# Optimization experiments

Measured on AMD Instinct MI355X. Metric: run time of the kernel, lower is better.

The kernel has to match this reference:

```python
import jax, jax.numpy as jnp
import numpy as np
from jax import lax

G, N, S, K, R = 8, 4096, 2048, 64, 0.4   # graphs, nodes/graph, fps samples (ratio=0.5), max neighbors, radius
EPER = 65536                              # edges per graph (avg degree 16)
C = 13                                    # num_classes


def setup_inputs():
    key = jax.random.key(0)
    ks = jax.random.split(key, 8)
    norm = jax.random.normal(ks[0], (G * N, 3), jnp.float32)
    pos = jax.random.uniform(ks[1], (G * N, 3), jnp.float32)
    x = jax.random.normal(ks[2], (G * N, 2), jnp.float32)
    e = jax.random.randint(ks[3], (2, G, EPER), 0, N)
    off = (jnp.arange(G) * N)[None, :, None]
    edge_index = (e + off).reshape(2, G * EPER).astype(jnp.int64)
    batch = jnp.repeat(jnp.arange(G), N).astype(jnp.int64)
    def lin(k, i, o):
        return jax.random.normal(k, (i, o), jnp.float32) / np.float32(np.sqrt(i))
    W1 = lin(ks[4], 8, 64);    b1 = jnp.zeros((64,), jnp.float32)
    W2 = lin(ks[5], 72, 128);  b2 = jnp.zeros((128,), jnp.float32)
    W3 = lin(ks[6], 139, 256); b3 = jnp.zeros((256,), jnp.float32)
    lin_w = lin(ks[7], 256, C); lin_b = jnp.zeros((C,), jnp.float32)
    return dict(norm=norm, pos=pos, x=x, edge_index=edge_index, batch=batch,
                W1=W1, b1=b1, W2=W2, b2=b2, W3=W3, b3=b3, lin_w=lin_w, lin_b=lin_b)


def _gcn(h, src, dst, ew, W, b, n):
    # GCNConv(normalize=False): out[dst] += ew * (h @ W)[src]; + bias
    m = (h @ W)[src] * ew[:, None]
    return jax.ops.segment_sum(m, dst, num_segments=n) + b


def _fps(p):  # farthest point sampling on one graph, p: [N,3] -> [S] local indices (start at node 0)
    def step(carry, _):
        mind, cur = carry
        d = jnp.sum((p - p[cur]) ** 2, axis=1)
        mind = jnp.minimum(mind, d)
        return (mind, jnp.argmax(mind).astype(jnp.int32)), cur
    _, idx = lax.scan(step, (jnp.full((N,), jnp.inf, p.dtype), jnp.int32(0)), None, length=S)
    return idx


def _radius(p, q):  # p [N,3], q [S,3] -> neighbor cols [S,K] (lowest-index-first within radius), valid mask
    d2 = jnp.sum((q[:, None, :] - p[None, :, :]) ** 2, axis=-1)  # [S,N]
    mask = d2 < R * R
    score = jnp.where(mask, N - jnp.arange(N, dtype=jnp.int32)[None, :], 0)
    vals, cols = lax.top_k(score, K)
    valid = vals > 0
    return jnp.where(valid, cols, 0), valid


def reference(norm, pos, x, edge_index, batch, W1, b1, W2, b2, W3, b3, lin_w, lin_b):
    NT = G * N
    inp = jnp.concatenate([norm, pos, x], axis=1)          # [NT, 8]
    src, dst = edge_index[0], edge_index[1]
    ew = jnp.ones((src.shape[0],), inp.dtype)
    # dropout is inactive at inference (training=False)
    h1 = jax.nn.relu(_gcn(inp, src, dst, ew, W1, b1, NT))  # [NT, 64]
    h1 = jnp.concatenate([h1, inp], axis=1)                # [NT, 72]
    h2 = jax.nn.relu(_gcn(h1, src, dst, ew, W2, b2, NT))   # [NT, 128]

    pg = pos.reshape(G, N, 3)
    pgs = lax.stop_gradient(pg)
    idx_loc = jax.vmap(_fps)(pgs)                          # [G, S] local indices
    q = jax.vmap(lambda p, i: p[i])(pg, idx_loc)           # [G, S, 3] sampled positions
    cols, valid = jax.vmap(_radius)(pgs, lax.stop_gradient(q))  # [G, S, K]

    # PointConv with identity local_nn/global_nn: max over neighbors of [x_j, pos_j - pos_i]
    hg = h2.reshape(G, N, 128)
    def pconv(h, p, qv, c, v):
        msg = jnp.concatenate([h[c], p[c] - qv[:, None, :]], axis=-1)  # [S, K, 131]
        msg = jnp.where(v[..., None], msg, -jnp.inf)
        return jnp.max(msg, axis=1)                                    # [S, 131]
    x_int = jax.vmap(pconv)(hg, pg, q, cols, valid).reshape(G * S, 131)

    # filter_adj: keep edges with both endpoints sampled, remap to new ids
    idx_flat = (idx_loc + (jnp.arange(G) * N)[:, None]).reshape(-1)    # [G*S] global indices
    mapping = jnp.full((NT,), -1, jnp.int32).at[idx_flat].set(jnp.arange(G * S, dtype=jnp.int32))
    ns, nd = mapping[src], mapping[dst]
    em = (ns >= 0) & (nd >= 0)
    ew3 = em.astype(inp.dtype)
    ns = jnp.where(em, ns, 0)
    nd = jnp.where(em, nd, 0)

    h3in = jnp.concatenate([x_int, inp[idx_flat]], axis=1)  # [G*S, 139]
    h3 = jax.nn.relu(_gcn(h3in, ns, nd, ew3, W3, b3, G * S))  # [G*S, 256]

    pooled = h3.reshape(G, S, 256).max(axis=1)              # global_max_pool -> [G, 256]
    logits = pooled @ lin_w + lin_b
    out = jax.nn.log_softmax(logits, axis=1)
    pred = jax.nn.softmax(out, axis=1)
    return (out, pred)
```

## Files before the change

### kernel.cpp

```cpp
#include <hip/hip_runtime.h>
#include <hip/hip_bf16.h>

constexpr int NG   = 8;
constexpr int NPG  = 4096;
constexpr int NT   = NG * NPG;
constexpr int NS   = 2048;
constexpr int GS   = NG * NS;
constexpr int KN   = 64;
constexpr int NE   = NG * 65536;
constexpr int NC   = 13;
constexpr int NWORK = 248;

__device__ __forceinline__ float inp_val(const float* norm, const float* pos, const float* x,
                                         int node, int dim) {
  if (dim < 3) return norm[(size_t)node * 3 + dim];
  if (dim < 6) return pos[(size_t)node * 3 + (dim - 3)];
  return x[(size_t)node * 2 + (dim - 6)];
}

__device__ __forceinline__ void wbar(int* ctrs, int k, int target) {
  __syncthreads();
  __threadfence();
  if (threadIdx.x == 0) {
    __hip_atomic_fetch_add(&ctrs[k], 1, __ATOMIC_RELEASE, __HIP_MEMORY_SCOPE_AGENT);
    while (__hip_atomic_load(&ctrs[k], __ATOMIC_ACQUIRE, __HIP_MEMORY_SCOPE_AGENT) < target)
      __builtin_amdgcn_s_sleep(16);
  }
  __syncthreads();
}

__global__ __launch_bounds__(256, 1) void phaseA_kernel(
    const float* __restrict__ pos, int* __restrict__ idxf, float* __restrict__ qpos,
    const float* __restrict__ norm, const float* __restrict__ x,
    const float* __restrict__ W1, float* __restrict__ t1,
    const int* __restrict__ ei, int* __restrict__ deg,
    int* __restrict__ off1, int* __restrict__ cur1, int* __restrict__ el1,
    const float* __restrict__ b1, const float* __restrict__ W2, float* __restrict__ t2,
    const float* __restrict__ b2, float* __restrict__ h2,
    int* __restrict__ wctr) {
  if (blockIdx.x >= 8) {
    const int wb = blockIdx.x - 8;
    const int sub = threadIdx.x >> 6;
    const int f = threadIdx.x & 63;
    __shared__ float wrow[4][80];
    __shared__ int sscan[256];
    for (int n0 = wb * 4; n0 < NT; n0 += NWORK * 4) {
      int n = n0 + sub;
      if (f < 8) wrow[sub][f] = inp_val(norm, pos, x, n, f);
      float acc = 0.f;
#pragma unroll
      for (int i = 0; i < 8; ++i) acc += wrow[sub][i] * W1[i * 64 + f];
      t1[(size_t)n * 64 + f] = acc;
    }
    for (int e = wb * 256 + threadIdx.x; e < NE; e += NWORK * 256)
      atomicAdd(&deg[ei[NE + e]], 1);
    wbar(wctr, 0, NWORK);
    if (wb == 0) {
      int t = threadIdx.x, base = t * 128, s = 0;
      for (int i = 0; i < 128; ++i) s += deg[base + i];
      sscan[t] = s;
      __syncthreads();
      for (int d = 1; d < 256; d <<= 1) {
        int v = (t >= d) ? sscan[t - d] : 0;
        __syncthreads();
        sscan[t] += v;
        __syncthreads();
      }
      int excl = (t == 0) ? 0 : sscan[t - 1];
      for (int i = 0; i < 128; ++i) { off1[base + i] = excl; excl += deg[base + i]; }
      if (t == 255) off1[NT] = sscan[255];
    }
    wbar(wctr, 1, NWORK);
    for (int e = wb * 256 + threadIdx.x; e < NE; e += NWORK * 256) {
      int sN = ei[e], dN = ei[NE + e];
      int p = off1[dN] + atomicAdd(&cur1[dN], 1);
      el1[p] = sN;
    }
    wbar(wctr, 2, NWORK);
    for (int n0 = wb * 4; n0 < NT; n0 += NWORK * 4) {
      int n = n0 + sub;
      int e0 = off1[n], e1 = off1[n + 1];
      float acc = 0.f;
      for (int j = e0; j < e1; ++j) acc += t1[(size_t)el1[j] * 64 + f];
      wrow[sub][f] = fmaxf(acc + b1[f], 0.f);
      if (f < 8) wrow[sub][64 + f] = inp_val(norm, pos, x, n, f);
      float a0 = 0.f, a1 = 0.f;
#pragma unroll 8
      for (int i = 0; i < 72; ++i) {
        float r = wrow[sub][i];
        a0 += r * W2[i * 128 + f];
        a1 += r * W2[i * 128 + 64 + f];
      }
      t2[(size_t)n * 128 + f] = a0;
      t2[(size_t)n * 128 + 64 + f] = a1;
    }
    wbar(wctr, 3, NWORK);
    {
      const int f2 = threadIdx.x & 127, sub2 = threadIdx.x >> 7;
      for (int n0 = wb * 2; n0 < NT; n0 += NWORK * 2) {
        int n = n0 + sub2;
        int e0 = off1[n], e1 = off1[n + 1];
        float acc = 0.f;
        for (int j = e0; j < e1; ++j) acc += t2[(size_t)el1[j] * 128 + f2];
        h2[(size_t)n * 128 + f2] = fmaxf(acc + b2[f2], 0.f);
      }
    }
    return;
  }
  const int g = blockIdx.x;
  __shared__ float4 sq[2][4];
  __shared__ int sidx[2][4];
  __shared__ float4 qrec[NS];
  __shared__ int irec[NS];
  const float* pg = pos + (size_t)g * NPG * 3;
  const int tid = threadIdx.x;
  const int wave = tid >> 6, lane = tid & 63;
  const int p0 = tid * 16;

  float a[48];
  {
    const float4* pg4 = reinterpret_cast<const float4*>(pg + (size_t)p0 * 3);
#pragma unroll
    for (int j = 0; j < 12; ++j) {
      float4 t = pg4[j];
      a[4 * j + 0] = t.x; a[4 * j + 1] = t.y; a[4 * j + 2] = t.z; a[4 * j + 3] = t.w;
    }
  }
  float px[16], py[16], pz[16], mind[16];
#pragma unroll
  for (int i = 0; i < 16; ++i) {
    px[i] = a[3 * i]; py[i] = a[3 * i + 1]; pz[i] = a[3 * i + 2];
    mind[i] = __int_as_float(0x7f800000);
  }
  float cx = pg[0], cy = pg[1], cz = pg[2];
  int idx_sel = 0;

  for (int s = 0; s < NS; ++s) {
    if (tid == 0) { irec[s] = idx_sel; qrec[s] = make_float4(cx, cy, cz, 0.f); }
    float bestv = -1.f, bx = 0.f, by = 0.f, bz = 0.f;
    int bi = 0;
#pragma unroll
    for (int i = 0; i < 16; ++i) {
      float dx = __fsub_rn(px[i], cx);
      float dy = __fsub_rn(py[i], cy);
      float dz = __fsub_rn(pz[i], cz);
      float dd = __fadd_rn(__fadd_rn(__fmul_rn(dx, dx), __fmul_rn(dy, dy)), __fmul_rn(dz, dz));
      float nm = fminf(mind[i], dd);
      mind[i] = nm;
      bool gt = nm > bestv;
      bestv = gt ? nm : bestv;
      bx = gt ? px[i] : bx;
      by = gt ? py[i] : by;
      bz = gt ? pz[i] : bz;
      bi = gt ? i : bi;
    }
    float v = bestv;
    v = fmaxf(v, __int_as_float(__builtin_amdgcn_update_dpp(0, __float_as_int(v), 0x111, 0xF, 0xF, true)));
    v = fmaxf(v, __int_as_float(__builtin_amdgcn_update_dpp(0, __float_as_int(v), 0x112, 0xF, 0xF, true)));
    v = fmaxf(v, __int_as_float(__builtin_amdgcn_update_dpp(0, __float_as_int(v), 0x114, 0xF, 0xF, true)));
    v = fmaxf(v, __int_as_float(__builtin_amdgcn_update_dpp(0, __float_as_int(v), 0x118, 0xF, 0xF, true)));
    v = fmaxf(v, __int_as_float(__builtin_amdgcn_update_dpp(0, __float_as_int(v), 0x142, 0xF, 0xF, true)));
    v = fmaxf(v, __int_as_float(__builtin_amdgcn_update_dpp(0, __float_as_int(v), 0x143, 0xF, 0xF, true)));
    int maxbits = __builtin_amdgcn_readlane(__float_as_int(v), 63);
    float wavemax = __int_as_float(maxbits);
    unsigned long long ball = __ballot(bestv == wavemax);
    int winner = __ffsll(ball) - 1;
    int b = s & 1;
    if (lane == winner) {
      sq[b][wave] = make_float4(bx, by, bz, wavemax);
      sidx[b][wave] = p0 + bi;
    }
    __syncthreads();
    float4 q0 = sq[b][0], q1 = sq[b][1], q2 = sq[b][2], q3 = sq[b][3];
    float4 qs = q3;
    if (q2.w >= qs.w) qs = q2;
    if (q1.w >= qs.w) qs = q1;
    if (q0.w >= qs.w) qs = q0;
    cx = qs.x; cy = qs.y; cz = qs.z;
    if (tid == 0) {
      int i0 = sidx[b][0], i1 = sidx[b][1], i2 = sidx[b][2], i3 = sidx[b][3];
      float r = q3.w; int is = i3;
      if (q2.w >= r) { r = q2.w; is = i2; }
      if (q1.w >= r) { r = q1.w; is = i1; }
      if (q0.w >= r) { r = q0.w; is = i0; }
      idx_sel = is;
    }
  }
  __syncthreads();
  for (int j = tid; j < NS; j += 256) {
    idxf[g * NS + j] = g * NPG + irec[j];
    float4 q = qrec[j];
    size_t m = (size_t)(g * NS + j) * 3;
    qpos[m + 0] = q.x; qpos[m + 1] = q.y; qpos[m + 2] = q.z;
  }
}

__global__ void featdeg_kernel(const float* __restrict__ xint, const int* __restrict__ idxf,
                               const float* __restrict__ norm, const float* __restrict__ pos,
                               const float* __restrict__ x, const float* __restrict__ W3,
                               float* __restrict__ t3,
                               const int* __restrict__ ei, const int* __restrict__ mp,
                               int* __restrict__ deg) {
  if (blockIdx.x >= GS) {
    int e = (blockIdx.x - GS) * 256 + threadIdx.x;
    int ns = mp[ei[e]], nd = mp[ei[NE + e]];
    if (ns >= 0 && nd >= 0) atomicAdd(&deg[nd], 1);
    return;
  }
  int m = blockIdx.x, f = threadIdx.x;
  __shared__ float row[139];
  if (f < 131) row[f] = xint[(size_t)m * 131 + f];
  else if (f < 139) { int node = idxf[m]; row[f] = inp_val(norm, pos, x, node, f - 131); }
  __syncthreads();
  float acc = 0.f;
#pragma unroll 8
  for (int i = 0; i < 139; ++i) acc += row[i] * W3[i * 256 + f];
  t3[(size_t)m * 256 + f] = acc;
}

__global__ void fill2_kernel(const int* __restrict__ ei, const int* __restrict__ mp,
                             const int* __restrict__ off, int* __restrict__ cur,
                             int* __restrict__ el) {
  int e = blockIdx.x * 256 + threadIdx.x;
  if (e < NE) {
    int ns = mp[ei[e]], nd = mp[ei[NE + e]];
    if (ns >= 0 && nd >= 0) {
      int p = off[nd] + atomicAdd(&cur[nd], 1);
      el[p] = ns;
    }
  }
}

__global__ __launch_bounds__(1024) void scan_kernel(const int* __restrict__ in,
                                                    int* __restrict__ out, int n) {
  __shared__ int ls[1024];
  int tid = threadIdx.x;
  int per = (n + 1023) >> 10;
  int base = tid * per;
  int s = 0;
  for (int i = 0; i < per; ++i) { int idx = base + i; if (idx < n) s += in[idx]; }
  ls[tid] = s;
  __syncthreads();
  for (int d = 1; d < 1024; d <<= 1) {
    int v = (tid >= d) ? ls[tid - d] : 0;
    __syncthreads();
    ls[tid] += v;
    __syncthreads();
  }
  int excl = (tid == 0) ? 0 : ls[tid - 1];
  for (int i = 0; i < per; ++i) {
    int idx = base + i;
    if (idx < n) { out[idx] = excl; excl += in[idx]; }
  }
  if (tid == 1023) out[n] = ls[1023];
}

__global__ void agg_kernel(const float* __restrict__ t, const int* __restrict__ off,
                           const int* __restrict__ el, const float* __restrict__ b,
                           float* __restrict__ out, int F) {
  int node = blockIdx.x, f = threadIdx.x;
  int e0 = off[node], e1 = off[node + 1];
  float acc = 0.f;
  for (int j = e0; j < e1; ++j) acc += t[(size_t)el[j] * F + f];
  out[(size_t)node * F + f] = fmaxf(acc + b[f], 0.f);
}

__global__ __launch_bounds__(256) void radius_kernel(const float* __restrict__ pos,
                                                     const float* __restrict__ qpos,
                                                     int* __restrict__ cols,
                                                     int* __restrict__ cnt,
                                                     const int* __restrict__ idxf,
                                                     int* __restrict__ mp) {
  const int g = blockIdx.x;
  __shared__ float sx[NPG], sy[NPG], sz[NPG];
  const float* pg = pos + (size_t)g * NPG * 3;
  for (int i = threadIdx.x; i < NPG * 3; i += 256) {
    float v = pg[i]; int node = i / 3, c = i - node * 3;
    if (c == 0) sx[node] = v; else if (c == 1) sy[node] = v; else sz[node] = v;
  }
  __syncthreads();
  int m = g * NS + blockIdx.y * 256 + threadIdx.x;
  mp[idxf[m]] = m;
  float qx = qpos[(size_t)m * 3], qy = qpos[(size_t)m * 3 + 1], qz = qpos[(size_t)m * 3 + 2];
  int* out = cols + (size_t)m * KN;
  int c = 0;
  for (int i = 0; i < NPG; ++i) {
    float dx = __fsub_rn(sx[i], qx);
    float dy = __fsub_rn(sy[i], qy);
    float dz = __fsub_rn(sz[i], qz);
    float d2 = __fadd_rn(__fadd_rn(__fmul_rn(dx, dx), __fmul_rn(dy, dy)), __fmul_rn(dz, dz));
    if (d2 < 0.16f) {
      out[c++] = i;
      if (c == KN) break;
    }
  }
  cnt[m] = c;
}

__global__ __launch_bounds__(64) void pointconv_kernel(const float* __restrict__ h2,
                                                       const float* __restrict__ pos,
                                                       const float* __restrict__ qpos,
                                                       const int* __restrict__ cols,
                                                       const int* __restrict__ cnt,
                                                       float* __restrict__ xint) {
  int m = blockIdx.x, t = threadIdx.x;
  int g = m / NS;
  int n = cnt[m];
  const int* cl = cols + (size_t)m * KN;
  float m0 = -INFINITY, m1 = -INFINITY, mp = -INFINITY;
  for (int k = 0; k < n; ++k) {
    int c = cl[k];
    size_t base = (size_t)(g * NPG + c);
    m0 = fmaxf(m0, h2[base * 128 + t]);
    m1 = fmaxf(m1, h2[base * 128 + 64 + t]);
    if (t < 3) mp = fmaxf(mp, pos[base * 3 + t]);
  }
  float* xo = xint + (size_t)m * 131;
  xo[t] = m0;
  xo[64 + t] = m1;
  if (t < 3) xo[128 + t] = __fsub_rn(mp, qpos[(size_t)m * 3 + t]);
}

__global__ void pool_kernel(const float* __restrict__ h3, float* __restrict__ pooled) {
  int g = blockIdx.x, ch = blockIdx.y, f = threadIdx.x;
  float mx = 0.f;
  size_t base = ((size_t)g * NS + (size_t)ch * 256) * 256 + f;
  for (int s = 0; s < 256; ++s) mx = fmaxf(mx, h3[base + (size_t)s * 256]);
  atomicMax((int*)pooled + g * 256 + f, __float_as_int(mx));
}

__global__ void head_kernel(const float* __restrict__ pooled, const float* __restrict__ lw,
                            const float* __restrict__ lb, float* __restrict__ outp) {
  __shared__ float lg[NG * NC];
  int t = threadIdx.x;
  if (t < NG * NC) {
    int g = t / NC, c = t % NC;
    float acc = lb[c];
    for (int k = 0; k < 256; ++k) acc += pooled[g * 256 + k] * lw[k * NC + c];
    lg[t] = acc;
  }
  __syncthreads();
  if (t < NG) {
    int g = t;
    float mx = -INFINITY;
    for (int c = 0; c < NC; ++c) mx = fmaxf(mx, lg[g * NC + c]);
    float sum = 0.f;
    for (int c = 0; c < NC; ++c) sum += expf(lg[g * NC + c] - mx);
    float lse = logf(sum);
    float ov[NC];
    float mx2 = -INFINITY;
    for (int c = 0; c < NC; ++c) {
      ov[c] = lg[g * NC + c] - mx - lse;
      outp[g * NC + c] = ov[c];
      mx2 = fmaxf(mx2, ov[c]);
    }
    float s2 = 0.f;
    for (int c = 0; c < NC; ++c) s2 += expf(ov[c] - mx2);
    for (int c = 0; c < NC; ++c) outp[NG * NC + g * NC + c] = expf(ov[c] - mx2) / s2;
  }
}

extern "C" void kernel_launch(void* const* d_in, const int* in_sizes, int n_in,
                              void* d_out, int out_size, void* d_ws, size_t ws_size,
                              hipStream_t stream) {
  const float* norm = (const float*)d_in[0];
  const float* pos  = (const float*)d_in[1];
  const float* x    = (const float*)d_in[2];
  const int* ei     = (const int*)d_in[3];
  const float* W1 = (const float*)d_in[5];
  const float* b1 = (const float*)d_in[6];
  const float* W2 = (const float*)d_in[7];
  const float* b2 = (const float*)d_in[8];
  const float* W3 = (const float*)d_in[9];
  const float* b3 = (const float*)d_in[10];
  const float* lw = (const float*)d_in[11];
  const float* lb = (const float*)d_in[12];
  float* outp = (float*)d_out;

  char* w = (char*)d_ws;
  size_t o = 0;
  auto alloc = [&](size_t bytes) -> void* {
    void* p = w + o;
    o = (o + bytes + 255) & ~(size_t)255;
    return p;
  };
  float* A    = (float*)alloc((size_t)NT * 128 * 4);
  float* Bf   = (float*)alloc((size_t)NT * 128 * 4);
  float* T1   = (float*)alloc((size_t)NT * 64 * 4);
  float* xint = (float*)alloc((size_t)GS * 131 * 4);
  int* cols   = (int*)alloc((size_t)GS * KN * 4);
  int* cnt    = (int*)alloc((size_t)GS * 4);
  int* deg1   = (int*)alloc((size_t)NT * 4);
  int* off1   = (int*)alloc((size_t)(NT + 1) * 4);
  int* cur1   = (int*)alloc((size_t)NT * 4);
  int* el1    = (int*)alloc((size_t)NE * 4);
  int* deg2   = (int*)alloc((size_t)GS * 4);
  int* off2   = (int*)alloc((size_t)(GS + 1) * 4);
  int* cur2   = (int*)alloc((size_t)GS * 4);
  int* el2    = (int*)alloc((size_t)NE * 4);
  int* idxf   = (int*)alloc((size_t)GS * 4);
  float* qpos = (float*)alloc((size_t)GS * 3 * 4);
  int* mapv   = (int*)alloc((size_t)NT * 4);
  float* pooled = (float*)alloc((size_t)NG * 256 * 4);
  int* wctr   = (int*)alloc(64);

  hipMemsetAsync(deg1, 0, (size_t)NT * 4, stream);
  hipMemsetAsync(cur1, 0, (size_t)NT * 4, stream);
  hipMemsetAsync(deg2, 0, (size_t)GS * 4, stream);
  hipMemsetAsync(cur2, 0, (size_t)GS * 4, stream);
  hipMemsetAsync(mapv, 0xFF, (size_t)NT * 4, stream);
  hipMemsetAsync(pooled, 0, (size_t)NG * 256 * 4, stream);
  hipMemsetAsync(wctr, 0, 64, stream);

  {
    void* ka[] = {(void*)&pos, (void*)&idxf, (void*)&qpos, (void*)&norm, (void*)&x,
                  (void*)&W1, (void*)&T1, (void*)&ei, (void*)&deg1,
                  (void*)&off1, (void*)&cur1, (void*)&el1,
                  (void*)&b1, (void*)&W2, (void*)&A, (void*)&b2, (void*)&Bf,
                  (void*)&wctr};
    hipLaunchCooperativeKernel((const void*)phaseA_kernel, dim3(8 + NWORK), dim3(256),
                               ka, 0, stream);
  }
  radius_kernel<<<dim3(NG, NS / 256), 256, 0, stream>>>(pos, qpos, cols, cnt, idxf, mapv);
  pointconv_kernel<<<GS, 64, 0, stream>>>(Bf, pos, qpos, cols, cnt, xint);
  featdeg_kernel<<<GS + NE / 256, 256, 0, stream>>>(xint, idxf, norm, pos, x, W3, A,
                                                    ei, mapv, deg2);
  scan_kernel<<<1, 1024, 0, stream>>>(deg2, off2, GS);
  fill2_kernel<<<NE / 256, 256, 0, stream>>>(ei, mapv, off2, cur2, el2);
  agg_kernel<<<GS, 256, 0, stream>>>(A, off2, el2, b3, Bf, 256);
  pool_kernel<<<dim3(NG, NS / 256), 256, 0, stream>>>(Bf, pooled);
  head_kernel<<<1, 128, 0, stream>>>(pooled, lw, lb, outp);
}
```

Measured before the change: 2.166 ms.

## Fuse radius search and point conv into cooperative kernel, streaming FPS output

The FPS blocks now publish sampled indices and query positions every 64 samples, with a per-graph progress counter. Worker blocks, once done with the GCN phases, dynamically grab 256-query chunks and wait on that counter, so the radius search runs while FPS is still going. Each chunk then does the point-conv max aggregation using neighbor lists kept in shared memory rather than global cols/cnt buffers. This removes two kernel launches and the neighbor-list round trip through global memory. In exchange, shared memory grows to about 113 KB per block, and the FPS critical path gains periodic fences and syncs.

```diff
diff --git a/kernel.cpp b/kernel.cpp
--- a/kernel.cpp
+++ b/kernel.cpp
@@ -37,13 +37,15 @@
     int* __restrict__ off1, int* __restrict__ cur1, int* __restrict__ el1,
     const float* __restrict__ b1, const float* __restrict__ W2, float* __restrict__ t2,
     const float* __restrict__ b2, float* __restrict__ h2,
+    int* __restrict__ mapv, float* __restrict__ xint,
     int* __restrict__ wctr) {
+  __shared__ __align__(16) char smem[115728];
   if (blockIdx.x >= 8) {
     const int wb = blockIdx.x - 8;
     const int sub = threadIdx.x >> 6;
     const int f = threadIdx.x & 63;
-    __shared__ float wrow[4][80];
-    __shared__ int sscan[256];
+    float (*wrow)[80] = (float (*)[80])smem;
+    int* sscan = (int*)(smem + 1280);
     for (int n0 = wb * 4; n0 < NT; n0 += NWORK * 4) {
       int n = n0 + sub;
       if (f < 8) wrow[sub][f] = inp_val(norm, pos, x, n, f);
@@ -105,13 +107,81 @@
         h2[(size_t)n * 128 + f2] = fmaxf(acc + b2[f2], 0.f);
       }
     }
+    wbar(wctr, 4, NWORK);
+    {
+      float* spx = (float*)smem;
+      float* spy = (float*)(smem + 16384);
+      float* spz = (float*)(smem + 32768);
+      int (*scolsT)[256] = (int (*)[256])(smem + 49152);
+      int* scnt = (int*)(smem + 114688);
+      int* schunk = (int*)(smem + 115712);
+      for (;;) {
+        if (threadIdx.x == 0)
+          *schunk = __hip_atomic_fetch_add(&wctr[8], 1, __ATOMIC_RELAXED,
+                                           __HIP_MEMORY_SCOPE_AGENT);
+        __syncthreads();
+        int chunk = *schunk;
+        __syncthreads();
+        if (chunk >= 64) break;
+        int gC = chunk >> 3, c0 = (chunk & 7) * 256;
+        const float* pgc = pos + (size_t)gC * NPG * 3;
+        for (int i = threadIdx.x; i < NPG * 3; i += 256) {
+          float v = pgc[i]; int node = i / 3, cc = i - node * 3;
+          if (cc == 0) spx[node] = v; else if (cc == 1) spy[node] = v; else spz[node] = v;
+        }
+        if (threadIdx.x == 0) {
+          while (__hip_atomic_load(&wctr[16 + gC], __ATOMIC_ACQUIRE,
+                                   __HIP_MEMORY_SCOPE_AGENT) < c0 + 256)
+            __builtin_amdgcn_s_sleep(32);
+        }
+        __syncthreads();
+        {
+          int m = gC * NS + c0 + threadIdx.x;
+          mapv[idxf[m]] = m;
+          float qx = qpos[(size_t)m * 3], qy = qpos[(size_t)m * 3 + 1],
+                qz = qpos[(size_t)m * 3 + 2];
+          int c = 0;
+          for (int i = 0; i < NPG; ++i) {
+            float dx = __fsub_rn(spx[i], qx);
+            float dy = __fsub_rn(spy[i], qy);
+            float dz = __fsub_rn(spz[i], qz);
+            float d2 = __fadd_rn(__fadd_rn(__fmul_rn(dx, dx), __fmul_rn(dy, dy)),
+                                 __fmul_rn(dz, dz));
+            if (d2 < 0.16f) {
+              scolsT[c][threadIdx.x] = i;
+              if (++c == KN) break;
+            }
+          }
+          scnt[threadIdx.x] = c;
+        }
+        __syncthreads();
+        for (int ss = (threadIdx.x >> 6); ss < 256; ss += 4) {
+          int fc = threadIdx.x & 63;
+          int m = gC * NS + c0 + ss;
+          int n = scnt[ss];
+          float m0 = -INFINITY, m1 = -INFINITY, mpv = -INFINITY;
+          for (int k = 0; k < n; ++k) {
+            int cc = scolsT[k][ss];
+            size_t b = (size_t)(gC * NPG + cc);
+            m0 = fmaxf(m0, h2[b * 128 + fc]);
+            m1 = fmaxf(m1, h2[b * 128 + 64 + fc]);
+            if (fc < 3) mpv = fmaxf(mpv, (fc == 0 ? spx[cc] : (fc == 1 ? spy[cc] : spz[cc])));
+          }
+          float* xo = xint + (size_t)m * 131;
+          xo[fc] = m0;
+          xo[64 + fc] = m1;
+          if (fc < 3) xo[128 + fc] = __fsub_rn(mpv, qpos[(size_t)m * 3 + fc]);
+        }
+        __syncthreads();
+      }
+    }
     return;
   }
   const int g = blockIdx.x;
-  __shared__ float4 sq[2][4];
-  __shared__ int sidx[2][4];
-  __shared__ float4 qrec[NS];
-  __shared__ int irec[NS];
+  float4* qrec = (float4*)smem;
+  int* irec = (int*)(smem + 32768);
+  float4 (*sq)[4] = (float4 (*)[4])(smem + 40960);
+  int (*sidx)[4] = (int (*)[4])(smem + 41088);
   const float* pg = pos + (size_t)g * NPG * 3;
   const int tid = threadIdx.x;
   const int wave = tid >> 6, lane = tid & 63;
@@ -185,13 +255,16 @@
       if (q0.w >= r) { r = q0.w; is = i0; }
       idx_sel = is;
     }
-  }
-  __syncthreads();
-  for (int j = tid; j < NS; j += 256) {
-    idxf[g * NS + j] = g * NPG + irec[j];
-    float4 q = qrec[j];
-    size_t m = (size_t)(g * NS + j) * 3;
-    qpos[m + 0] = q.x; qpos[m + 1] = q.y; qpos[m + 2] = q.z;
+    if ((s & 63) == 63) {
+      int smp = (s - 63) + (tid >> 2);
+      int comp = tid & 3;
+      if (comp < 3) qpos[(size_t)(g * NS + smp) * 3 + comp] = ((float*)&qrec[smp])[comp];
+      else idxf[g * NS + smp] = g * NPG + irec[smp];
+      __threadfence();
+      __syncthreads();
+      if (tid == 0)
+        __hip_atomic_store(&wctr[16 + g], s + 1, __ATOMIC_RELEASE, __HIP_MEMORY_SCOPE_AGENT);
+    }
   }
 }
 
@@ -263,62 +336,6 @@
   float acc = 0.f;
   for (int j = e0; j < e1; ++j) acc += t[(size_t)el[j] * F + f];
   out[(size_t)node * F + f] = fmaxf(acc + b[f], 0.f);
-}
-
-__global__ __launch_bounds__(256) void radius_kernel(const float* __restrict__ pos,
-                                                     const float* __restrict__ qpos,
-                                                     int* __restrict__ cols,
-                                                     int* __restrict__ cnt,
-                                                     const int* __restrict__ idxf,
-                                                     int* __restrict__ mp) {
-  const int g = blockIdx.x;
-  __shared__ float sx[NPG], sy[NPG], sz[NPG];
-  const float* pg = pos + (size_t)g * NPG * 3;
-  for (int i = threadIdx.x; i < NPG * 3; i += 256) {
-    float v = pg[i]; int node = i / 3, c = i - node * 3;
-    if (c == 0) sx[node] = v; else if (c == 1) sy[node] = v; else sz[node] = v;
-  }
-  __syncthreads();
-  int m = g * NS + blockIdx.y * 256 + threadIdx.x;
-  mp[idxf[m]] = m;
-  float qx = qpos[(size_t)m * 3], qy = qpos[(size_t)m * 3 + 1], qz = qpos[(size_t)m * 3 + 2];
-  int* out = cols + (size_t)m * KN;
-  int c = 0;
-  for (int i = 0; i < NPG; ++i) {
-    float dx = __fsub_rn(sx[i], qx);
-    float dy = __fsub_rn(sy[i], qy);
-    float dz = __fsub_rn(sz[i], qz);
-    float d2 = __fadd_rn(__fadd_rn(__fmul_rn(dx, dx), __fmul_rn(dy, dy)), __fmul_rn(dz, dz));
-    if (d2 < 0.16f) {
-      out[c++] = i;
-      if (c == KN) break;
-    }
-  }
-  cnt[m] = c;
-}
-
-__global__ __launch_bounds__(64) void pointconv_kernel(const float* __restrict__ h2,
-                                                       const float* __restrict__ pos,
-                                                       const float* __restrict__ qpos,
-                                                       const int* __restrict__ cols,
-                                                       const int* __restrict__ cnt,
-                                                       float* __restrict__ xint) {
-  int m = blockIdx.x, t = threadIdx.x;
-  int g = m / NS;
-  int n = cnt[m];
-  const int* cl = cols + (size_t)m * KN;
-  float m0 = -INFINITY, m1 = -INFINITY, mp = -INFINITY;
-  for (int k = 0; k < n; ++k) {
-    int c = cl[k];
-    size_t base = (size_t)(g * NPG + c);
-    m0 = fmaxf(m0, h2[base * 128 + t]);
-    m1 = fmaxf(m1, h2[base * 128 + 64 + t]);
-    if (t < 3) mp = fmaxf(mp, pos[base * 3 + t]);
-  }
-  float* xo = xint + (size_t)m * 131;
-  xo[t] = m0;
-  xo[64 + t] = m1;
-  if (t < 3) xo[128 + t] = __fsub_rn(mp, qpos[(size_t)m * 3 + t]);
 }
 
 __global__ void pool_kernel(const float* __restrict__ h3, float* __restrict__ pooled) {
@@ -388,8 +405,6 @@
   float* Bf   = (float*)alloc((size_t)NT * 128 * 4);
   float* T1   = (float*)alloc((size_t)NT * 64 * 4);
   float* xint = (float*)alloc((size_t)GS * 131 * 4);
-  int* cols   = (int*)alloc((size_t)GS * KN * 4);
-  int* cnt    = (int*)alloc((size_t)GS * 4);
   int* deg1   = (int*)alloc((size_t)NT * 4);
   int* off1   = (int*)alloc((size_t)(NT + 1) * 4);
   int* cur1   = (int*)alloc((size_t)NT * 4);
@@ -402,7 +417,7 @@
   float* qpos = (float*)alloc((size_t)GS * 3 * 4);
   int* mapv   = (int*)alloc((size_t)NT * 4);
   float* pooled = (float*)alloc((size_t)NG * 256 * 4);
-  int* wctr   = (int*)alloc(64);
+  int* wctr   = (int*)alloc(128);
 
   hipMemsetAsync(deg1, 0, (size_t)NT * 4, stream);
   hipMemsetAsync(cur1, 0, (size_t)NT * 4, stream);
@@ -410,19 +425,17 @@
   hipMemsetAsync(cur2, 0, (size_t)GS * 4, stream);
   hipMemsetAsync(mapv, 0xFF, (size_t)NT * 4, stream);
   hipMemsetAsync(pooled, 0, (size_t)NG * 256 * 4, stream);
-  hipMemsetAsync(wctr, 0, 64, stream);
+  hipMemsetAsync(wctr, 0, 128, stream);
 
   {
     void* ka[] = {(void*)&pos, (void*)&idxf, (void*)&qpos, (void*)&norm, (void*)&x,
                   (void*)&W1, (void*)&T1, (void*)&ei, (void*)&deg1,
                   (void*)&off1, (void*)&cur1, (void*)&el1,
                   (void*)&b1, (void*)&W2, (void*)&A, (void*)&b2, (void*)&Bf,
-                  (void*)&wctr};
+                  (void*)&mapv, (void*)&xint, (void*)&wctr};
     hipLaunchCooperativeKernel((const void*)phaseA_kernel, dim3(8 + NWORK), dim3(256),
                                ka, 0, stream);
   }
-  radius_kernel<<<dim3(NG, NS / 256), 256, 0, stream>>>(pos, qpos, cols, cnt, idxf, mapv);
-  pointconv_kernel<<<GS, 64, 0, stream>>>(Bf, pos, qpos, cols, cnt, xint);
   featdeg_kernel<<<GS + NE / 256, 256, 0, stream>>>(xint, idxf, norm, pos, x, W3, A,
                                                     ei, mapv, deg2);
   scan_kernel<<<1, 1024, 0, stream>>>(deg2, off2, GS);
```

After: 2.726 ms. 25.9% more time.

## Keep worker blocks spinning during FPS and reuse W3 across four rows

Applied to the files above, without the earlier changes.

The cooperative phase-A kernel now reserves about 84 KB of shared memory per block, so only one block fits per CU. Once worker blocks finish the GCN stages, they no longer exit; they spin on an FMA busy loop until all eight FPS blocks signal completion through a new counter. The likely aim is to keep other blocks off the FPS CUs, or to hold the GPU clock state, while the serial farthest-point-sampling loop runs; the cost is extra power draw, which could lower clocks instead. Separately, the W3 feature transform now computes four rows per block, so each W3 load is reused four times and the block count drops.

```diff
diff --git a/kernel.cpp b/kernel.cpp
--- a/kernel.cpp
+++ b/kernel.cpp
@@ -10,6 +10,7 @@
 constexpr int NE   = NG * 65536;
 constexpr int NC   = 13;
 constexpr int NWORK = 248;
+constexpr int NF3B = 4096;
 
 __device__ __forceinline__ float inp_val(const float* norm, const float* pos, const float* x,
                                          int node, int dim) {
@@ -38,12 +39,13 @@
     const float* __restrict__ b1, const float* __restrict__ W2, float* __restrict__ t2,
     const float* __restrict__ b2, float* __restrict__ h2,
     int* __restrict__ wctr) {
+  __shared__ __align__(16) char smem[84000];
   if (blockIdx.x >= 8) {
     const int wb = blockIdx.x - 8;
     const int sub = threadIdx.x >> 6;
     const int f = threadIdx.x & 63;
-    __shared__ float wrow[4][80];
-    __shared__ int sscan[256];
+    float (*wrow)[80] = (float (*)[80])smem;
+    int* sscan = (int*)(smem + 1280);
     for (int n0 = wb * 4; n0 < NT; n0 += NWORK * 4) {
       int n = n0 + sub;
       if (f < 8) wrow[sub][f] = inp_val(norm, pos, x, n, f);
@@ -105,13 +107,20 @@
         h2[(size_t)n * 128 + f2] = fmaxf(acc + b2[f2], 0.f);
       }
     }
+    {
+      float r0 = 1.f + (float)threadIdx.x * 1e-6f;
+      while (__hip_atomic_load(&wctr[9], __ATOMIC_ACQUIRE, __HIP_MEMORY_SCOPE_AGENT) < 8) {
+        for (int it = 0; it < 4096; ++it) r0 = __fmaf_rn(r0, 1.0000001f, 1e-7f);
+      }
+      if (r0 == 123.456f) t1[0] = r0;
+    }
     return;
   }
   const int g = blockIdx.x;
-  __shared__ float4 sq[2][4];
-  __shared__ int sidx[2][4];
-  __shared__ float4 qrec[NS];
-  __shared__ int irec[NS];
+  float4* qrec = (float4*)smem;
+  int* irec = (int*)(smem + 32768);
+  float4 (*sq)[4] = (float4 (*)[4])(smem + 40960);
+  int (*sidx)[4] = (int (*)[4])(smem + 41088);
   const float* pg = pos + (size_t)g * NPG * 3;
   const int tid = threadIdx.x;
   const int wave = tid >> 6, lane = tid & 63;
@@ -193,76 +202,10 @@
     size_t m = (size_t)(g * NS + j) * 3;
     qpos[m + 0] = q.x; qpos[m + 1] = q.y; qpos[m + 2] = q.z;
   }
-}
-
-__global__ void featdeg_kernel(const float* __restrict__ xint, const int* __restrict__ idxf,
-                               const float* __restrict__ norm, const float* __restrict__ pos,
-                               const float* __restrict__ x, const float* __restrict__ W3,
-                               float* __restrict__ t3,
-                               const int* __restrict__ ei, const int* __restrict__ mp,
-                               int* __restrict__ deg) {
-  if (blockIdx.x >= GS) {
-    int e = (blockIdx.x - GS) * 256 + threadIdx.x;
-    int ns = mp[ei[e]], nd = mp[ei[NE + e]];
-    if (ns >= 0 && nd >= 0) atomicAdd(&deg[nd], 1);
-    return;
-  }
-  int m = blockIdx.x, f = threadIdx.x;
-  __shared__ float row[139];
-  if (f < 131) row[f] = xint[(size_t)m * 131 + f];
-  else if (f < 139) { int node = idxf[m]; row[f] = inp_val(norm, pos, x, node, f - 131); }
-  __syncthreads();
-  float acc = 0.f;
-#pragma unroll 8
-  for (int i = 0; i < 139; ++i) acc += row[i] * W3[i * 256 + f];
-  t3[(size_t)m * 256 + f] = acc;
-}
-
-__global__ void fill2_kernel(const int* __restrict__ ei, const int* __restrict__ mp,
-                             const int* __restrict__ off, int* __restrict__ cur,
-                             int* __restrict__ el) {
-  int e = blockIdx.x * 256 + threadIdx.x;
-  if (e < NE) {
-    int ns = mp[ei[e]], nd = mp[ei[NE + e]];
-    if (ns >= 0 && nd >= 0) {
-      int p = off[nd] + atomicAdd(&cur[nd], 1);
-      el[p] = ns;
-    }
-  }
-}
-
-__global__ __launch_bounds__(1024) void scan_kernel(const int* __restrict__ in,
-                                                    int* __restrict__ out, int n) {
-  __shared__ int ls[1024];
-  int tid = threadIdx.x;
-  int per = (n + 1023) >> 10;
-  int base = tid * per;
-  int s = 0;
-  for (int i = 0; i < per; ++i) { int idx = base + i; if (idx < n) s += in[idx]; }
-  ls[tid] = s;
-  __syncthreads();
-  for (int d = 1; d < 1024; d <<= 1) {
-    int v = (tid >= d) ? ls[tid - d] : 0;
-    __syncthreads();
-    ls[tid] += v;
-    __syncthreads();
-  }
-  int excl = (tid == 0) ? 0 : ls[tid - 1];
-  for (int i = 0; i < per; ++i) {
-    int idx = base + i;
-    if (idx < n) { out[idx] = excl; excl += in[idx]; }
-  }
-  if (tid == 1023) out[n] = ls[1023];
-}
-
-__global__ void agg_kernel(const float* __restrict__ t, const int* __restrict__ off,
-                           const int* __restrict__ el, const float* __restrict__ b,
-                           float* __restrict__ out, int F) {
-  int node = blockIdx.x, f = threadIdx.x;
-  int e0 = off[node], e1 = off[node + 1];
-  float acc = 0.f;
-  for (int j = e0; j < e1; ++j) acc += t[(size_t)el[j] * F + f];
-  out[(size_t)node * F + f] = fmaxf(acc + b[f], 0.f);
+  __threadfence();
+  __syncthreads();
+  if (tid == 0)
+    __hip_atomic_fetch_add(&wctr[9], 1, __ATOMIC_RELEASE, __HIP_MEMORY_SCOPE_AGENT);
 }
 
 __global__ __launch_bounds__(256) void radius_kernel(const float* __restrict__ pos,
@@ -319,6 +262,90 @@
   xo[t] = m0;
   xo[64 + t] = m1;
   if (t < 3) xo[128 + t] = __fsub_rn(mp, qpos[(size_t)m * 3 + t]);
+}
+
+__global__ void post2_kernel(const float* __restrict__ xint, const int* __restrict__ idxf,
+                             const float* __restrict__ norm, const float* __restrict__ pos,
+                             const float* __restrict__ x, const float* __restrict__ W3,
+                             float* __restrict__ t3,
+                             const int* __restrict__ ei, const int* __restrict__ mp,
+                             int* __restrict__ deg) {
+  if (blockIdx.x >= NF3B) {
+    int e = (blockIdx.x - NF3B) * 256 + threadIdx.x;
+    int ns = mp[ei[e]], nd = mp[ei[NE + e]];
+    if (ns >= 0 && nd >= 0) atomicAdd(&deg[nd], 1);
+    return;
+  }
+  __shared__ float srow[4][140];
+  const int m0 = blockIdx.x * 4;
+  for (int j = threadIdx.x; j < 4 * 139; j += 256) {
+    int sub = j / 139, i = j - sub * 139;
+    int m = m0 + sub;
+    srow[sub][i] = (i < 131) ? xint[(size_t)m * 131 + i]
+                             : inp_val(norm, pos, x, idxf[m], i - 131);
+  }
+  __syncthreads();
+  int f = threadIdx.x;
+  float a0 = 0.f, a1 = 0.f, a2 = 0.f, a3 = 0.f;
+#pragma unroll 8
+  for (int i = 0; i < 139; ++i) {
+    float wv = W3[i * 256 + f];
+    a0 += srow[0][i] * wv;
+    a1 += srow[1][i] * wv;
+    a2 += srow[2][i] * wv;
+    a3 += srow[3][i] * wv;
+  }
+  t3[(size_t)(m0 + 0) * 256 + f] = a0;
+  t3[(size_t)(m0 + 1) * 256 + f] = a1;
+  t3[(size_t)(m0 + 2) * 256 + f] = a2;
+  t3[(size_t)(m0 + 3) * 256 + f] = a3;
+}
+
+__global__ void fill2_kernel(const int* __restrict__ ei, const int* __restrict__ mp,
+                             const int* __restrict__ off, int* __restrict__ cur,
+                             int* __restrict__ el) {
+  int e = blockIdx.x * 256 + threadIdx.x;
+  if (e < NE) {
+    int ns = mp[ei[e]], nd = mp[ei[NE + e]];
+    if (ns >= 0 && nd >= 0) {
+      int p = off[nd] + atomicAdd(&cur[nd], 1);
+      el[p] = ns;
+    }
+  }
+}
+
+__global__ __launch_bounds__(1024) void scan_kernel(const int* __restrict__ in,
+                                                    int* __restrict__ out, int n) {
+  __shared__ int ls[1024];
+  int tid = threadIdx.x;
+  int per = (n + 1023) >> 10;
+  int base = tid * per;
+  int s = 0;
+  for (int i = 0; i < per; ++i) { int idx = base + i; if (idx < n) s += in[idx]; }
+  ls[tid] = s;
+  __syncthreads();
+  for (int d = 1; d < 1024; d <<= 1) {
+    int v = (tid >= d) ? ls[tid - d] : 0;
+    __syncthreads();
+    ls[tid] += v;
+    __syncthreads();
+  }
+  int excl = (tid == 0) ? 0 : ls[tid - 1];
+  for (int i = 0; i < per; ++i) {
+    int idx = base + i;
+    if (idx < n) { out[idx] = excl; excl += in[idx]; }
+  }
+  if (tid == 1023) out[n] = ls[1023];
+}
+
+__global__ void agg_kernel(const float* __restrict__ t, const int* __restrict__ off,
+                           const int* __restrict__ el, const float* __restrict__ b,
+                           float* __restrict__ out, int F) {
+  int node = blockIdx.x, f = threadIdx.x;
+  int e0 = off[node], e1 = off[node + 1];
+  float acc = 0.f;
+  for (int j = e0; j < e1; ++j) acc += t[(size_t)el[j] * F + f];
+  out[(size_t)node * F + f] = fmaxf(acc + b[f], 0.f);
 }
 
 __global__ void pool_kernel(const float* __restrict__ h3, float* __restrict__ pooled) {
@@ -402,7 +429,7 @@
   float* qpos = (float*)alloc((size_t)GS * 3 * 4);
   int* mapv   = (int*)alloc((size_t)NT * 4);
   float* pooled = (float*)alloc((size_t)NG * 256 * 4);
-  int* wctr   = (int*)alloc(64);
+  int* wctr   = (int*)alloc(128);
 
   hipMemsetAsync(deg1, 0, (size_t)NT * 4, stream);
   hipMemsetAsync(cur1, 0, (size_t)NT * 4, stream);
@@ -410,7 +437,7 @@
   hipMemsetAsync(cur2, 0, (size_t)GS * 4, stream);
   hipMemsetAsync(mapv, 0xFF, (size_t)NT * 4, stream);
   hipMemsetAsync(pooled, 0, (size_t)NG * 256 * 4, stream);
-  hipMemsetAsync(wctr, 0, 64, stream);
+  hipMemsetAsync(wctr, 0, 128, stream);
 
   {
     void* ka[] = {(void*)&pos, (void*)&idxf, (void*)&qpos, (void*)&norm, (void*)&x,
@@ -423,7 +450,7 @@
   }
   radius_kernel<<<dim3(NG, NS / 256), 256, 0, stream>>>(pos, qpos, cols, cnt, idxf, mapv);
   pointconv_kernel<<<GS, 64, 0, stream>>>(Bf, pos, qpos, cols, cnt, xint);
-  featdeg_kernel<<<GS + NE / 256, 256, 0, stream>>>(xint, idxf, norm, pos, x, W3, A,
+  post2_kernel<<<NF3B + NE / 256, 256, 0, stream>>>(xint, idxf, norm, pos, x, W3, A,
                                                     ei, mapv, deg2);
   scan_kernel<<<1, 1024, 0, stream>>>(deg2, off2, GS);
   fill2_kernel<<<NE / 256, 256, 0, stream>>>(ei, mapv, off2, cur2, el2);
```

Result: no change. 2.153 ms (-0.6%).
